# Kernel tuning notes

Measured on AMD Instinct MI355X. Metric: run time of the kernel, lower is better.

The kernel has to match this reference:

```python
import jax, jax.numpy as jnp
import numpy as np

F, D = 4, 64          # n_facet, emb_dim
FD = F * D            # cur_dim = 256
NITER = 3             # args.iter

def _embed(x, W, b):
    # SparseInputLinear: torch.mm(x, weight) + bias
    return x @ W + b

def _homo(self_e, neigh_e, a):
    # HomoAttention(emb_dim, n_facet): per-facet gated fusion of self and neighbor embeds
    B = self_e.shape[0]
    s = self_e.reshape(B, F, D)
    n = neigh_e.reshape(B, F, D)
    score = jax.nn.leaky_relu(jnp.concatenate([s, n], axis=-1) @ a, 0.2)  # [B,F]
    alpha = jax.nn.sigmoid(score)[..., None]
    return (s + alpha * n).reshape(B, FD)

def _norm(x):
    return x / (jnp.linalg.norm(x, axis=-1, keepdims=True) + 1e-8)

def _hete(self_e, stacked):
    # HeteAttention(emb_dim, n_facet, niter): disentangled routing over K relation channels
    B, K = stacked.shape[0], stacked.shape[1]
    u0 = _norm(self_e.reshape(B, F, D))
    z = _norm(stacked.reshape(B, K, F, D))
    u = u0
    for _ in range(NITER):
        p = jax.nn.softmax(jnp.einsum('bfd,bkfd->bkf', u, z), axis=1)
        u = _norm(u0 + jnp.einsum('bkf,bkfd->bfd', p, z))
    return u.reshape(B, FD)

def setup_inputs() -> dict:
    key = jax.random.key(0)
    ks = jax.random.split(key, 32)
    B, NU, NB, NC, NG = 1024, 20000, 20000, 1000, 500
    def r(i, shape):
        return jax.random.uniform(ks[i], shape, dtype=jnp.float32)
    def p(i, shape, fan):
        s = 1.0 / np.sqrt(fan)
        return jax.random.uniform(ks[i], shape, minval=-s, maxval=s, dtype=jnp.float32)
    return {
        "users": r(0, (B, NU)), "businesses": r(1, (B, NB)),
        "u_neigh_user": r(2, (B, NU)), "u_neigh_business": r(3, (B, NB)),
        "u_neigh_city": r(4, (B, NC)), "u_neigh_category": r(5, (B, NG)),
        "b_neigh_user": r(6, (B, NU)), "b_neigh_business": r(7, (B, NB)),
        "b_neigh_city": r(8, (B, NC)), "b_neigh_category": r(9, (B, NG)),
        "W_user": p(10, (NU, FD), FD), "b_user": p(11, (FD,), FD),
        "W_bus": p(12, (NB, FD), FD), "b_bus": p(13, (FD,), FD),
        "W_city": p(14, (NC, FD), FD), "b_city": p(15, (FD,), FD),
        "W_cat": p(16, (NG, FD), FD), "b_cat": p(17, (FD,), FD),
        "homo_a": p(18, (8, 2 * D), 2 * D),
    }

def reference(users, businesses, u_neigh_user, u_neigh_business, u_neigh_city, u_neigh_category,
              b_neigh_user, b_neigh_business, b_neigh_city, b_neigh_category,
              W_user, b_user, W_bus, b_bus, W_city, b_city, W_cat, b_cat, homo_a):
    user_embed = _embed(users, W_user, b_user)
    business_embed = _embed(businesses, W_bus, b_bus)
    Ws = [(W_user, b_user), (W_bus, b_bus), (W_city, b_city), (W_cat, b_cat)]
    u_neighs = [u_neigh_user, u_neigh_business, u_neigh_city, u_neigh_category]
    b_neighs = [b_neigh_user, b_neigh_business, b_neigh_city, b_neigh_category]
    u_list = [_homo(user_embed, _embed(n, W, b), homo_a[i])
              for i, (n, (W, b)) in enumerate(zip(u_neighs, Ws))]
    updated_user = _hete(user_embed, jnp.stack(u_list, axis=1))
    b_list = [_homo(business_embed, _embed(n, W, b), homo_a[4 + i])
              for i, (n, (W, b)) in enumerate(zip(b_neighs, Ws))]
    # NOTE: original torch code passes user_embed (not business_embed) as the self
    # node to the business hete encoder; we reproduce that faithfully.
    updated_business = _hete(user_embed, jnp.stack(b_list, axis=1))
    # UserItemAttention / autocross: per-facet interaction logits, softmax over dim=1
    logit = jnp.einsum('bfd,bfd->bf',
                       updated_user.reshape(-1, F, D),
                       updated_business.reshape(-1, F, D))
    return jax.nn.softmax(logit, axis=1)
```

## Files before the change

kernel.cpp:

```cpp
#include <hip/hip_runtime.h>
#include <hip/hip_bf16.h>
#include <stdint.h>
#include <stddef.h>

typedef __attribute__((ext_vector_type(8))) _Float16 f16x8;
typedef __attribute__((ext_vector_type(4))) float f32x4;

#define B_ROWS 1024
#define ND 256

struct ConvArgs {
  const float* W[4];
  unsigned short* dst[4];
  int K[4];
  int chBase[4];
};

__global__ void conv_w_kernel(ConvArgs a){
  int cb = blockIdx.x;
  int w = 0;
  if (cb >= a.chBase[1]) w = 1;
  if (cb >= a.chBase[2]) w = 2;
  if (cb >= a.chBase[3]) w = 3;
  int c = cb - a.chBase[w];
  __shared__ float tile[32][257];
  const float* Wp = a.W[w];
  int K = a.K[w];
  int t = threadIdx.x;
  int r = t >> 3, c0 = (t & 7) * 32;
  int gk = c * 32 + r;
  if (gk < K){
    const float* src = Wp + (size_t)gk * ND + c0;
    #pragma unroll
    for (int j = 0; j < 32; j += 4){
      float4 v = *(const float4*)(src + j);
      tile[r][c0+j+0] = v.x; tile[r][c0+j+1] = v.y;
      tile[r][c0+j+2] = v.z; tile[r][c0+j+3] = v.w;
    }
  } else {
    #pragma unroll
    for (int j = 0; j < 32; ++j) tile[r][c0+j] = 0.f;
  }
  __syncthreads();
  int n = t;
  union { unsigned short s[32]; uint4 v[4]; } pk;
  #pragma unroll
  for (int k = 0; k < 32; ++k){
    _Float16 h = (_Float16)tile[k][n];
    pk.s[k] = *(unsigned short*)&h;
  }
  unsigned short* d = a.dst[w] + ((size_t)c * ND + n) * 32;
  #pragma unroll
  for (int q = 0; q < 4; ++q) *(uint4*)(d + q*8) = pk.v[q];
}

struct BiasArgs { float* emb; const float* b[10]; };

__global__ void bias_init_kernel(BiasArgs a){
  int idx = blockIdx.x * blockDim.x + threadIdx.x;
  int g  = idx >> 16;
  int wi = idx & 65535;
  int n4 = (wi & 63) * 4;
  const float* bp = a.b[g];
  float4 v; v.x = bp[n4]; v.y = bp[n4+1]; v.z = bp[n4+2]; v.w = bp[n4+3];
  *(float4*)(a.emb + (size_t)idx * 4) = v;
}

struct GemmArgs {
  const float* X[10];
  const unsigned short* Wh[10];
  float* C[10];
  int K[10];
  int nch[10];
  int ksplit[10];
  int wgBase[11];
};

__device__ __forceinline__ void load8(float* d, const float* p, int k0, int K){
  if (k0 + 8 <= K){
    float4 v0 = *(const float4*)(p + k0);
    float4 v1 = *(const float4*)(p + k0 + 4);
    d[0]=v0.x; d[1]=v0.y; d[2]=v0.z; d[3]=v0.w;
    d[4]=v1.x; d[5]=v1.y; d[6]=v1.z; d[7]=v1.w;
  } else {
    #pragma unroll
    for (int j = 0; j < 8; ++j) d[j] = (k0 + j < K) ? p[k0 + j] : 0.f;
  }
}

__launch_bounds__(256, 3)
__global__ void gemm_kernel(GemmArgs a){
  __shared__ _Float16 Ah[64][40];
  __shared__ _Float16 Al[64][40];

  int nx = (int)gridDim.x >> 3;
  int bid = ((int)blockIdx.x & 7) * nx + ((int)blockIdx.x >> 3);

  int g = 0;
  while (bid >= a.wgBase[g+1]) ++g;
  int loc = bid - a.wgBase[g];
  int mt = loc & 15;
  int ks = loc >> 4;
  int nch = a.nch[g], ksp = a.ksplit[g];
  int q = nch / ksp, r = nch % ksp;
  int c0  = ks * q + (ks < r ? ks : r);
  int cnt = q + (ks < r ? 1 : 0);

  const float* X = a.X[g];
  int K = a.K[g];
  const unsigned short* Wh = a.Wh[g];

  int t = threadIdx.x;
  int lane = t & 63, w = t >> 6;
  int ln15 = lane & 15, kg = lane >> 4;
  int rowbase = mt * 64;
  int srow = t >> 2, sk = (t & 3) * 8;
  const float* xrow = X + (size_t)(rowbase + srow) * K;

  f32x4 acc[4][4];
  #pragma unroll
  for (int i = 0; i < 4; ++i)
    #pragma unroll
    for (int j = 0; j < 4; ++j) acc[i][j] = (f32x4){0.f,0.f,0.f,0.f};

  float cur[8], nx1[8];
  load8(cur, xrow, c0*32 + sk, K);
  if (cnt > 1) load8(nx1, xrow, (c0+1)*32 + sk, K);

  for (int ci = 0; ci < cnt; ++ci){
    int c = c0 + ci;
    f16x8 bh[4];
    size_t cb = (size_t)c * (ND * 32);
    #pragma unroll
    for (int j = 0; j < 4; ++j)
      bh[j] = *(const f16x8*)(Wh + cb + (size_t)(w*64 + j*16 + ln15) * 32 + kg*8);
    float nx2[8];
    if (ci + 2 < cnt){
      load8(nx2, xrow, (c+2)*32 + sk, K);
    } else {
      for (int j = 0; j < 8; ++j) nx2[j] = 0.f;
    }
    union { _Float16 h[8]; uint4 u; } H, L;
    #pragma unroll
    for (int j = 0; j < 8; ++j){
      _Float16 h = (_Float16)cur[j];
      H.h[j] = h;
      L.h[j] = (_Float16)(cur[j] - (float)h);
    }
    __syncthreads();
    *(uint4*)&Ah[srow][sk] = H.u;
    *(uint4*)&Al[srow][sk] = L.u;
    __syncthreads();
    #pragma unroll
    for (int i = 0; i < 4; ++i){
      f16x8 ah = *(const f16x8*)&Ah[i*16 + ln15][kg*8];
      f16x8 al = *(const f16x8*)&Al[i*16 + ln15][kg*8];
      #pragma unroll
      for (int j = 0; j < 4; ++j){
        acc[i][j] = __builtin_amdgcn_mfma_f32_16x16x32_f16(ah, bh[j], acc[i][j], 0, 0, 0);
        acc[i][j] = __builtin_amdgcn_mfma_f32_16x16x32_f16(al, bh[j], acc[i][j], 0, 0, 0);
      }
    }
    #pragma unroll
    for (int j = 0; j < 8; ++j){ cur[j] = nx1[j]; nx1[j] = nx2[j]; }
  }

  float* C = a.C[g];
  int crow0 = kg * 4;
  #pragma unroll
  for (int i = 0; i < 4; ++i){
    #pragma unroll
    for (int j = 0; j < 4; ++j){
      int col = w*64 + j*16 + ln15;
      #pragma unroll
      for (int rr = 0; rr < 4; ++rr){
        int row = rowbase + i*16 + crow0 + rr;
        atomicAdd(&C[(size_t)row * ND + col], acc[i][j][rr]);
      }
    }
  }
}

__device__ __forceinline__ float wsum(float v){
  #pragma unroll
  for (int m = 32; m; m >>= 1) v += __shfl_xor(v, m, 64);
  return v;
}

__global__ void fuse_kernel(const float* __restrict__ emb,
                            const float* __restrict__ homo_a,
                            float* __restrict__ out){
  int b = blockIdx.x;
  int t = threadIdx.x;
  int f = t >> 6;
  int d = t & 63;
  auto E = [&](int g){ return emb[((size_t)g * B_ROWS + b) * ND + t]; };

  float us = E(0), bs = E(1);
  float un[4], bn[4];
  #pragma unroll
  for (int i = 0; i < 4; ++i){ un[i] = E(2+i); bn[i] = E(6+i); }

  float ul[4], blv[4];
  #pragma unroll
  for (int i = 0; i < 4; ++i){
    float as_ = homo_a[i*128 + d],     an_ = homo_a[i*128 + 64 + d];
    float sc  = wsum(us*as_ + un[i]*an_);
    sc = sc > 0.f ? sc : 0.2f*sc;
    float alp = 1.f / (1.f + expf(-sc));
    ul[i] = us + alp*un[i];
    float as2 = homo_a[(4+i)*128 + d], an2 = homo_a[(4+i)*128 + 64 + d];
    float sc2 = wsum(bs*as2 + bn[i]*an2);
    sc2 = sc2 > 0.f ? sc2 : 0.2f*sc2;
    float alp2 = 1.f / (1.f + expf(-sc2));
    blv[i] = bs + alp2*bn[i];
  }

  float u0 = us / (sqrtf(wsum(us*us)) + 1e-8f);
  float zu[4], zb[4];
  #pragma unroll
  for (int i = 0; i < 4; ++i){
    zu[i] = ul[i]  / (sqrtf(wsum(ul[i]*ul[i]))   + 1e-8f);
    zb[i] = blv[i] / (sqrtf(wsum(blv[i]*blv[i])) + 1e-8f);
  }

  auto route = [&](float z0, float z1, float z2, float z3)->float{
    float u = u0;
    #pragma unroll
    for (int it = 0; it < 3; ++it){
      float d0 = wsum(u*z0), d1 = wsum(u*z1), d2 = wsum(u*z2), d3 = wsum(u*z3);
      float m = fmaxf(fmaxf(d0,d1), fmaxf(d2,d3));
      float e0 = expf(d0-m), e1 = expf(d1-m), e2 = expf(d2-m), e3 = expf(d3-m);
      float s = e0+e1+e2+e3;
      float nu = u0 + (e0*z0 + e1*z1 + e2*z2 + e3*z3) / s;
      u = nu / (sqrtf(wsum(nu*nu)) + 1e-8f);
    }
    return u;
  };

  float uu = route(zu[0], zu[1], zu[2], zu[3]);
  float ub = route(zb[0], zb[1], zb[2], zb[3]);

  float lg = wsum(uu*ub);
  __shared__ float sl[4];
  if (d == 0) sl[f] = lg;
  __syncthreads();
  if (t < 4){
    float l0 = sl[0], l1 = sl[1], l2 = sl[2], l3 = sl[3];
    float m = fmaxf(fmaxf(l0,l1), fmaxf(l2,l3));
    float den = expf(l0-m) + expf(l1-m) + expf(l2-m) + expf(l3-m);
    out[(size_t)b*4 + t] = expf(sl[t]-m) / den;
  }
}

extern "C" void kernel_launch(void* const* d_in, const int* in_sizes, int n_in,
                              void* d_out, int out_size, void* d_ws, size_t ws_size,
                              hipStream_t stream) {
  const float* X[10];
  for (int i = 0; i < 10; ++i) X[i] = (const float*)d_in[i];
  const float* Wm[4]   = { (const float*)d_in[10], (const float*)d_in[12],
                           (const float*)d_in[14], (const float*)d_in[16] };
  const float* bias[4] = { (const float*)d_in[11], (const float*)d_in[13],
                           (const float*)d_in[15], (const float*)d_in[17] };
  const float* homo_a  = (const float*)d_in[18];
  float* out = (float*)d_out;

  const size_t EMB_FLOATS = 10ull * B_ROWS * ND;
  float* emb = (float*)d_ws;
  unsigned short* wch = (unsigned short*)((char*)d_ws + EMB_FLOATS * 4);
  const int nchW[4] = {625, 625, 32, 16};
  const int Kw[4]   = {20000, 20000, 1000, 500};
  size_t off[4];
  {
    size_t o = 0;
    for (int w = 0; w < 4; ++w){ off[w] = o; o += (size_t)nchW[w] * ND * 32; }
  }

  ConvArgs ca;
  int cbase = 0;
  for (int w = 0; w < 4; ++w){
    ca.W[w] = Wm[w];
    ca.dst[w] = wch + off[w];
    ca.K[w] = Kw[w];
    ca.chBase[w] = cbase;
    cbase += nchW[w];
  }
  hipLaunchKernelGGL(conv_w_kernel, dim3(cbase), dim3(256), 0, stream, ca);

  static const int biasOf[10] = {0,1,0,1,2,3,0,1,2,3};
  BiasArgs ba;
  ba.emb = emb;
  for (int g = 0; g < 10; ++g) ba.b[g] = bias[biasOf[g]];
  hipLaunchKernelGGL(bias_init_kernel, dim3((EMB_FLOATS/4)/256), dim3(256), 0, stream, ba);

  static const int wOf[10] = {0,1,0,1,2,3,0,1,2,3};
  static const int ksp[10] = {10,10,10,10,2,1,10,10,2,1};
  GemmArgs ga;
  int base = 0;
  for (int g = 0; g < 10; ++g){
    ga.X[g]  = X[g];
    ga.Wh[g] = wch + off[wOf[g]];
    ga.C[g]  = emb + (size_t)g * B_ROWS * ND;
    ga.K[g]  = Kw[wOf[g]];
    ga.nch[g] = nchW[wOf[g]];
    ga.ksplit[g] = ksp[g];
    ga.wgBase[g] = base;
    base += 16 * ksp[g];
  }
  ga.wgBase[10] = base;
  hipLaunchKernelGGL(gemm_kernel, dim3(base), dim3(256), 0, stream, ga);

  hipLaunchKernelGGL(fuse_kernel, dim3(B_ROWS), dim3(256), 0, stream, emb, homo_a, out);
}
```

Before: 601.3 us.

## Load GEMM A operand directly into registers, dropping LDS staging and barriers

```diff
diff --git a/kernel.cpp b/kernel.cpp
--- a/kernel.cpp
+++ b/kernel.cpp
@@ -27,19 +27,18 @@
   const float* Wp = a.W[w];
   int K = a.K[w];
   int t = threadIdx.x;
-  int r = t >> 3, c0 = (t & 7) * 32;
-  int gk = c * 32 + r;
-  if (gk < K){
-    const float* src = Wp + (size_t)gk * ND + c0;
-    #pragma unroll
-    for (int j = 0; j < 32; j += 4){
-      float4 v = *(const float4*)(src + j);
-      tile[r][c0+j+0] = v.x; tile[r][c0+j+1] = v.y;
-      tile[r][c0+j+2] = v.z; tile[r][c0+j+3] = v.w;
-    }
-  } else {
-    #pragma unroll
-    for (int j = 0; j < 32; ++j) tile[r][c0+j] = 0.f;
+  const float* src = Wp + (size_t)c * 32 * ND;
+  bool full = (c * 32 + 32 <= K);
+  #pragma unroll
+  for (int j = 0; j < 8; ++j){
+    int idx = j * 256 + t;
+    int row = idx >> 6;
+    int col = (idx & 63) * 4;
+    float4 v;
+    if (full || (c * 32 + row < K)) v = *(const float4*)(src + (size_t)idx * 4);
+    else { v.x = v.y = v.z = v.w = 0.f; }
+    tile[row][col+0] = v.x; tile[row][col+1] = v.y;
+    tile[row][col+2] = v.z; tile[row][col+3] = v.w;
   }
   __syncthreads();
   int n = t;
@@ -76,23 +75,26 @@
   int wgBase[11];
 };
 
-__device__ __forceinline__ void load8(float* d, const float* p, int k0, int K){
-  if (k0 + 8 <= K){
-    float4 v0 = *(const float4*)(p + k0);
-    float4 v1 = *(const float4*)(p + k0 + 4);
-    d[0]=v0.x; d[1]=v0.y; d[2]=v0.z; d[3]=v0.w;
-    d[4]=v1.x; d[5]=v1.y; d[6]=v1.z; d[7]=v1.w;
-  } else {
-    #pragma unroll
-    for (int j = 0; j < 8; ++j) d[j] = (k0 + j < K) ? p[k0 + j] : 0.f;
-  }
-}
-
-__launch_bounds__(256, 3)
+__device__ __forceinline__ void ld8(float* d, const float* p){
+  float4 v0 = *(const float4*)p;
+  float4 v1 = *(const float4*)(p + 4);
+  d[0]=v0.x; d[1]=v0.y; d[2]=v0.z; d[3]=v0.w;
+  d[4]=v1.x; d[5]=v1.y; d[6]=v1.z; d[7]=v1.w;
+}
+
+__device__ __forceinline__ void cvt_hilo(const float* A, f16x8& H, f16x8& L){
+  _Float16 hh[8], ll[8];
+  #pragma unroll
+  for (int j = 0; j < 8; ++j){
+    _Float16 h = (_Float16)A[j];
+    hh[j] = h;
+    ll[j] = (_Float16)(A[j] - (float)h);
+  }
+  H = *(f16x8*)hh; L = *(f16x8*)ll;
+}
+
+__launch_bounds__(256, 4)
 __global__ void gemm_kernel(GemmArgs a){
-  __shared__ _Float16 Ah[64][40];
-  __shared__ _Float16 Al[64][40];
-
   int nx = (int)gridDim.x >> 3;
   int bid = ((int)blockIdx.x & 7) * nx + ((int)blockIdx.x >> 3);
 
@@ -114,55 +116,65 @@
   int lane = t & 63, w = t >> 6;
   int ln15 = lane & 15, kg = lane >> 4;
   int rowbase = mt * 64;
-  int srow = t >> 2, sk = (t & 3) * 8;
-  const float* xrow = X + (size_t)(rowbase + srow) * K;
+  const float* xr = X + (size_t)(rowbase + ln15) * K + kg * 8;
+  const size_t rstep = (size_t)16 * K;
 
   f32x4 acc[4][4];
   #pragma unroll
   for (int i = 0; i < 4; ++i)
     #pragma unroll
     for (int j = 0; j < 4; ++j) acc[i][j] = (f32x4){0.f,0.f,0.f,0.f};
-
-  float cur[8], nx1[8];
-  load8(cur, xrow, c0*32 + sk, K);
-  if (cnt > 1) load8(nx1, xrow, (c0+1)*32 + sk, K);
 
   for (int ci = 0; ci < cnt; ++ci){
     int c = c0 + ci;
+    int k0 = c * 32;
     f16x8 bh[4];
     size_t cb = (size_t)c * (ND * 32);
     #pragma unroll
     for (int j = 0; j < 4; ++j)
       bh[j] = *(const f16x8*)(Wh + cb + (size_t)(w*64 + j*16 + ln15) * 32 + kg*8);
-    float nx2[8];
-    if (ci + 2 < cnt){
-      load8(nx2, xrow, (c+2)*32 + sk, K);
+    float A0[8], A1[8], A2[8], A3[8];
+    if (k0 + 32 <= K){
+      ld8(A0, xr + k0);
+      ld8(A1, xr + k0 + rstep);
+      ld8(A2, xr + k0 + 2*rstep);
+      ld8(A3, xr + k0 + 3*rstep);
     } else {
-      for (int j = 0; j < 8; ++j) nx2[j] = 0.f;
-    }
-    union { _Float16 h[8]; uint4 u; } H, L;
-    #pragma unroll
-    for (int j = 0; j < 8; ++j){
-      _Float16 h = (_Float16)cur[j];
-      H.h[j] = h;
-      L.h[j] = (_Float16)(cur[j] - (float)h);
-    }
-    __syncthreads();
-    *(uint4*)&Ah[srow][sk] = H.u;
-    *(uint4*)&Al[srow][sk] = L.u;
-    __syncthreads();
-    #pragma unroll
-    for (int i = 0; i < 4; ++i){
-      f16x8 ah = *(const f16x8*)&Ah[i*16 + ln15][kg*8];
-      f16x8 al = *(const f16x8*)&Al[i*16 + ln15][kg*8];
       #pragma unroll
-      for (int j = 0; j < 4; ++j){
-        acc[i][j] = __builtin_amdgcn_mfma_f32_16x16x32_f16(ah, bh[j], acc[i][j], 0, 0, 0);
-        acc[i][j] = __builtin_amdgcn_mfma_f32_16x16x32_f16(al, bh[j], acc[i][j], 0, 0, 0);
+      for (int j = 0; j < 8; ++j){
+        int k = k0 + kg*8 + j;
+        bool ok = k < K;
+        A0[j] = ok ? xr[k0 + j] : 0.f;
+        A1[j] = ok ? xr[k0 + rstep + j] : 0.f;
+        A2[j] = ok ? xr[k0 + 2*rstep + j] : 0.f;
+        A3[j] = ok ? xr[k0 + 3*rstep + j] : 0.f;
       }
     }
-    #pragma unroll
-    for (int j = 0; j < 8; ++j){ cur[j] = nx1[j]; nx1[j] = nx2[j]; }
+    f16x8 H, L;
+    cvt_hilo(A0, H, L);
+    #pragma unroll
+    for (int j = 0; j < 4; ++j){
+      acc[0][j] = __builtin_amdgcn_mfma_f32_16x16x32_f16(H, bh[j], acc[0][j], 0, 0, 0);
+      acc[0][j] = __builtin_amdgcn_mfma_f32_16x16x32_f16(L, bh[j], acc[0][j], 0, 0, 0);
+    }
+    cvt_hilo(A1, H, L);
+    #pragma unroll
+    for (int j = 0; j < 4; ++j){
+      acc[1][j] = __builtin_amdgcn_mfma_f32_16x16x32_f16(H, bh[j], acc[1][j], 0, 0, 0);
+      acc[1][j] = __builtin_amdgcn_mfma_f32_16x16x32_f16(L, bh[j], acc[1][j], 0, 0, 0);
+    }
+    cvt_hilo(A2, H, L);
+    #pragma unroll
+    for (int j = 0; j < 4; ++j){
+      acc[2][j] = __builtin_amdgcn_mfma_f32_16x16x32_f16(H, bh[j], acc[2][j], 0, 0, 0);
+      acc[2][j] = __builtin_amdgcn_mfma_f32_16x16x32_f16(L, bh[j], acc[2][j], 0, 0, 0);
+    }
+    cvt_hilo(A3, H, L);
+    #pragma unroll
+    for (int j = 0; j < 4; ++j){
+      acc[3][j] = __builtin_amdgcn_mfma_f32_16x16x32_f16(H, bh[j], acc[3][j], 0, 0, 0);
+      acc[3][j] = __builtin_amdgcn_mfma_f32_16x16x32_f16(L, bh[j], acc[3][j], 0, 0, 0);
+    }
   }
 
   float* C = a.C[g];
```

New measurement: 775.2 us. 1.29x slower.
